# Optimization experiments

Hardware: AMD Instinct MI355X
Metric: run time of the kernel (lower is better)

## Reference

```python
import jax, jax.numpy as jnp
import numpy as np

B, N, D = 4, 4096, 512
H = 8
HD = D // H  # 64


def setup_inputs() -> dict:
    key = jax.random.key(0)
    ks = jax.random.split(key, 9)
    s = 1.0 / np.sqrt(D)
    return {
        "x": jax.random.normal(ks[0], (B, N, D), dtype=jnp.float32),
        "Wq": jax.random.normal(ks[1], (D, D), dtype=jnp.float32) * s,
        "bq": jax.random.normal(ks[2], (D,), dtype=jnp.float32) * 0.01,
        "Wk": jax.random.normal(ks[3], (D, D), dtype=jnp.float32) * s,
        "bk": jax.random.normal(ks[4], (D,), dtype=jnp.float32) * 0.01,
        "Wv": jax.random.normal(ks[5], (D, D), dtype=jnp.float32) * s,
        "bv": jax.random.normal(ks[6], (D,), dtype=jnp.float32) * 0.01,
        "Wo": jax.random.normal(ks[7], (D, D), dtype=jnp.float32) * s,
        "bo": jax.random.normal(ks[8], (D,), dtype=jnp.float32) * 0.01,
    }


def reference(x, Wq, bq, Wk, bk, Wv, bv, Wo, bo):
    # projections -> [B, H, N, HD]
    def split_heads(t):
        return t.reshape(B, N, H, HD).transpose(0, 2, 1, 3)

    q = split_heads(x @ Wq.T + bq)
    k = split_heads(x @ Wk.T + bk)
    v = split_heads(x @ Wv.T + bv)

    scale = 1.0 / np.sqrt(HD).astype(np.float32)
    scores = jnp.einsum("bhqd,bhkd->bhqk", q, k) * scale  # [B,H,N,N]
    attn = jax.nn.softmax(scores, axis=-1)
    out = jnp.einsum("bhqk,bhkd->bhqd", attn, v)  # [B,H,N,HD]
    out = out.transpose(0, 2, 1, 3).reshape(B, N, D)
    return out @ Wo.T + bo
```

## Files before the change

### kernel.cpp

```cpp
#include <hip/hip_runtime.h>
#include <hip/hip_bf16.h>

#define BB 4
#define NN 4096
#define DD 512
#define HH 8
#define HD 64

typedef __attribute__((ext_vector_type(4))) float f32x4;
typedef __attribute__((ext_vector_type(16))) float f32x16;
typedef __attribute__((ext_vector_type(8))) short short8;
typedef __attribute__((ext_vector_type(4))) unsigned int uint4v;

static __device__ __forceinline__ unsigned short f2bf(float f) {
    unsigned int u = __float_as_uint(f);
    u += 0x7fff + ((u >> 16) & 1);
    return (unsigned short)(u >> 16);
}

__global__ void convert_bf16(const float* __restrict__ in,
                             unsigned short* __restrict__ out, int n) {
    int i = (blockIdx.x * blockDim.x + threadIdx.x) * 8;
    int stride = gridDim.x * blockDim.x * 8;
    for (; i + 7 < n; i += stride) {
        f32x4 a = *reinterpret_cast<const f32x4*>(in + i);
        f32x4 b = *reinterpret_cast<const f32x4*>(in + i + 4);
        short8 o;
        o[0] = (short)f2bf(a[0]); o[1] = (short)f2bf(a[1]);
        o[2] = (short)f2bf(a[2]); o[3] = (short)f2bf(a[3]);
        o[4] = (short)f2bf(b[0]); o[5] = (short)f2bf(b[1]);
        o[6] = (short)f2bf(b[2]); o[7] = (short)f2bf(b[3]);
        *reinterpret_cast<short8*>(out + i) = o;
    }
}

__global__ void convert_weights(const float* __restrict__ W0, const float* __restrict__ W1,
                                const float* __restrict__ W2, const float* __restrict__ W3,
                                unsigned short* __restrict__ out) {
    int which = blockIdx.x >> 7;
    const float* src = which == 0 ? W0 : which == 1 ? W1 : which == 2 ? W2 : W3;
    unsigned short* dst = out + (size_t)which * DD * DD;
    int i = ((blockIdx.x & 127) * blockDim.x + threadIdx.x) * 8;
    f32x4 a = *reinterpret_cast<const f32x4*>(src + i);
    f32x4 b = *reinterpret_cast<const f32x4*>(src + i + 4);
    short8 o;
    o[0] = (short)f2bf(a[0]); o[1] = (short)f2bf(a[1]);
    o[2] = (short)f2bf(a[2]); o[3] = (short)f2bf(a[3]);
    o[4] = (short)f2bf(b[0]); o[5] = (short)f2bf(b[1]);
    o[6] = (short)f2bf(b[2]); o[7] = (short)f2bf(b[3]);
    *reinterpret_cast<short8*>(dst + i) = o;
}

template <int OUT_BF16>
__global__ __launch_bounds__(256)
void gemm_bias(const unsigned short* __restrict__ A,
               const unsigned short* __restrict__ W,
               const float* __restrict__ bias,
               void* __restrict__ Cout, float scale) {
    __shared__ uint4 ldsA[128 * 4];
    __shared__ uint4 ldsB[128 * 4];
    const int t = threadIdx.x;
    const int lane = t & 63;
    const int w = t >> 6;
    const int wr = w >> 1, wc = w & 1;
    const int brow = (int)blockIdx.y * 128;
    const int bcol = (int)blockIdx.x * 128;
    const int l16 = lane & 15;
    const int lq = lane >> 4;

    f32x4 acc[4][4] = {};

    const int sr = t >> 1;
    const int c16 = (t & 1) * 2;

    for (int k0 = 0; k0 < 512; k0 += 32) {
        const uint4* gA = reinterpret_cast<const uint4*>(A + (size_t)(brow + sr) * 512 + k0 + c16 * 8);
        const uint4* gB = reinterpret_cast<const uint4*>(W + (size_t)(bcol + sr) * 512 + k0 + c16 * 8);
        uint4 a0 = gA[0], a1 = gA[1];
        uint4 b0 = gB[0], b1 = gB[1];
        __syncthreads();
        ldsA[(sr * 4 + c16) ^ (sr & 7)]     = a0;
        ldsA[(sr * 4 + c16 + 1) ^ (sr & 7)] = a1;
        ldsB[(sr * 4 + c16) ^ (sr & 7)]     = b0;
        ldsB[(sr * 4 + c16 + 1) ^ (sr & 7)] = b1;
        __syncthreads();
        short8 af[4], bfr[4];
#pragma unroll
        for (int m = 0; m < 4; ++m) {
            int ra = wr * 64 + m * 16 + l16;
            af[m] = *reinterpret_cast<short8*>(&ldsA[(ra * 4 + lq) ^ (ra & 7)]);
            int rb = wc * 64 + m * 16 + l16;
            bfr[m] = *reinterpret_cast<short8*>(&ldsB[(rb * 4 + lq) ^ (rb & 7)]);
        }
#pragma unroll
        for (int m = 0; m < 4; ++m)
#pragma unroll
            for (int n = 0; n < 4; ++n)
                acc[m][n] = __builtin_amdgcn_mfma_f32_16x16x32_bf16(af[m], bfr[n], acc[m][n], 0, 0, 0);
    }

#pragma unroll
    for (int m = 0; m < 4; ++m) {
        int row = brow + wr * 64 + m * 16 + lq * 4;
#pragma unroll
        for (int n = 0; n < 4; ++n) {
            int col = bcol + wc * 64 + n * 16 + l16;
            float bv = bias[col];
#pragma unroll
            for (int r = 0; r < 4; ++r) {
                float v = (acc[m][n][r] + bv) * scale;
                if (OUT_BF16) {
                    ((unsigned short*)Cout)[(size_t)(row + r) * 512 + col] = f2bf(v);
                } else {
                    ((float*)Cout)[(size_t)(row + r) * 512 + col] = v;
                }
            }
        }
    }
}

__global__ __launch_bounds__(256)
void transpose_v(const unsigned short* __restrict__ Vb, unsigned short* __restrict__ Vt) {
    __shared__ unsigned short tile[64][72];
    const int bh = blockIdx.y;
    const int b = bh >> 3, h = bh & 7;
    const int n0 = blockIdx.x * 64;
    const int t = threadIdx.x;
    {
        int r = t >> 2;
        int cs = (t & 3) * 16;
        const short8* src = reinterpret_cast<const short8*>(
            Vb + (size_t)(b * NN + n0 + r) * DD + h * HD + cs);
        short8 v0 = src[0], v1 = src[1];
#pragma unroll
        for (int j = 0; j < 8; ++j) {
            tile[r][cs + j]     = (unsigned short)v0[j];
            tile[r][cs + 8 + j] = (unsigned short)v1[j];
        }
    }
    __syncthreads();
    {
        int d = t >> 2;
        int ns = (t & 3) * 16;
        short8 o0, o1;
#pragma unroll
        for (int j = 0; j < 8; ++j) {
            o0[j] = (short)tile[ns + j][d];
            o1[j] = (short)tile[ns + 8 + j][d];
        }
        unsigned short* dst = Vt + ((size_t)bh * HD + d) * NN + n0 + ns;
        *reinterpret_cast<short8*>(dst)     = o0;
        *reinterpret_cast<short8*>(dst + 8) = o1;
    }
}

__global__ __launch_bounds__(256)
void flash_attn(const unsigned short* __restrict__ Qb,
                const unsigned short* __restrict__ Kb,
                const unsigned short* __restrict__ Vt,
                unsigned short* __restrict__ Ob) {
    __shared__ __align__(16) char lds[32768];
    const int t = threadIdx.x;
    const int lane = t & 63;
    const int w = t >> 6;
    const int nid = (blockIdx.x & 7) * 128 + (blockIdx.x >> 3);
    const int bh = nid >> 5;
    const int qb = nid & 31;
    const int b = bh >> 3, h = bh & 7;
    const int q0 = qb * 128 + w * 32;
    const int l32 = lane & 31;
    const int hi = lane >> 5;

    const int i8 = lane >> 3, g8 = lane & 7;

    const unsigned short* qptr = Qb + (size_t)(b * NN + q0 + l32) * DD + h * HD + hi * 8;
    short8 qf[4];
#pragma unroll
    for (int c = 0; c < 4; ++c)
        qf[c] = *reinterpret_cast<const short8*>(qptr + c * 16);

    short8 ones;
#pragma unroll
    for (int j = 0; j < 8; ++j) ones[j] = (short)0x3F80;

    const f32x16 Z = {};
    f32x16 OT0 = {}, OT1 = {}, OTS = {};

    int koff[8], voff[8];
#pragma unroll
    for (int sub = 0; sub < 2; ++sub) {
#pragma unroll
        for (int c = 0; c < 4; ++c) {
            int row = sub * 32 + l32;
            int g = (hi + 2 * c) ^ (row & 7) ^ ((row >> 3) & 7);
            koff[sub * 4 + c] = row * 128 + g * 16;
        }
#pragma unroll
        for (int dblk = 0; dblk < 2; ++dblk)
#pragma unroll
            for (int c2 = 0; c2 < 2; ++c2) {
                int row = dblk * 32 + l32;
                int g = ((sub << 2) + (c2 << 1) + hi) ^ (row & 7) ^ ((row >> 3) & 7);
                voff[sub * 4 + dblk * 2 + c2] = 8192 + row * 128 + g * 16;
            }
    }

    const int rowl0 = w * 16 + i8;
    const int rowl1 = w * 16 + 8 + i8;
    const int gs0 = (g8 ^ i8 ^ ((2 * w) & 7)) * 8;
    const int gs1 = (g8 ^ i8 ^ ((2 * w + 1) & 7)) * 8;
    const unsigned short* kp0 = Kb + (size_t)(b * NN + rowl0) * DD + h * HD + gs0;
    const unsigned short* kp1 = Kb + (size_t)(b * NN + rowl1) * DD + h * HD + gs1;
    const unsigned short* vp0 = Vt + ((size_t)bh * HD + rowl0) * NN + gs0;
    const unsigned short* vp1 = Vt + ((size_t)bh * HD + rowl1) * NN + gs1;

    auto STAGE = [&](int bb) {
        __builtin_amdgcn_global_load_lds(
            (const __attribute__((address_space(1))) void*)kp0,
            (__attribute__((address_space(3))) void*)(lds + bb + (w * 16) * 128), 16, 0, 0);
        __builtin_amdgcn_global_load_lds(
            (const __attribute__((address_space(1))) void*)kp1,
            (__attribute__((address_space(3))) void*)(lds + bb + (w * 16 + 8) * 128), 16, 0, 0);
        __builtin_amdgcn_global_load_lds(
            (const __attribute__((address_space(1))) void*)vp0,
            (__attribute__((address_space(3))) void*)(lds + bb + 8192 + (w * 16) * 128), 16, 0, 0);
        __builtin_amdgcn_global_load_lds(
            (const __attribute__((address_space(1))) void*)vp1,
            (__attribute__((address_space(3))) void*)(lds + bb + 8192 + (w * 16 + 8) * 128), 16, 0, 0);
        kp0 += 64 * DD; kp1 += 64 * DD; vp0 += 64; vp1 += 64;
    };

    auto softpack = [&](const f32x16& S, short8& pa, short8& pb) {
        unsigned int wq[8];
#pragma unroll
        for (int j = 0; j < 8; ++j) {
            float p0 = __builtin_exp2f(S[2 * j]);
            float p1 = __builtin_exp2f(S[2 * j + 1]);
            asm("v_cvt_pk_bf16_f32 %0, %1, %2" : "=v"(wq[j]) : "v"(p0), "v"(p1));
        }
        asm("v_permlane32_swap_b32 %0, %1" : "+v"(wq[0]), "+v"(wq[2]));
        asm("v_permlane32_swap_b32 %0, %1" : "+v"(wq[1]), "+v"(wq[3]));
        asm("v_permlane32_swap_b32 %0, %1" : "+v"(wq[4]), "+v"(wq[6]));
        asm("v_permlane32_swap_b32 %0, %1" : "+v"(wq[5]), "+v"(wq[7]));
        uint4v pu0 = {wq[0], wq[1], wq[2], wq[3]};
        uint4v pu1 = {wq[4], wq[5], wq[6], wq[7]};
        pa = __builtin_bit_cast(short8, pu0);
        pb = __builtin_bit_cast(short8, pu1);
    };

    STAGE(0);
    __syncthreads();

    for (int it = 0; it < 32; ++it) {
#pragma unroll
        for (int half = 0; half < 2; ++half) {
            const int BO = half ? 16384 : 0;
            if (half == 0 || it != 31) STAGE(half ? 0 : 16384);

            short8 kf[8];
#pragma unroll
            for (int i = 0; i < 8; ++i)
                kf[i] = *reinterpret_cast<const short8*>(lds + BO + koff[i]);

            f32x16 S0, S1;
            S0 = __builtin_amdgcn_mfma_f32_32x32x16_bf16(kf[0], qf[0], Z, 0, 0, 0);
            S1 = __builtin_amdgcn_mfma_f32_32x32x16_bf16(kf[4], qf[0], Z, 0, 0, 0);
            S0 = __builtin_amdgcn_mfma_f32_32x32x16_bf16(kf[1], qf[1], S0, 0, 0, 0);
            S1 = __builtin_amdgcn_mfma_f32_32x32x16_bf16(kf[5], qf[1], S1, 0, 0, 0);
            S0 = __builtin_amdgcn_mfma_f32_32x32x16_bf16(kf[2], qf[2], S0, 0, 0, 0);
            S1 = __builtin_amdgcn_mfma_f32_32x32x16_bf16(kf[6], qf[2], S1, 0, 0, 0);
            S0 = __builtin_amdgcn_mfma_f32_32x32x16_bf16(kf[3], qf[3], S0, 0, 0, 0);
            S1 = __builtin_amdgcn_mfma_f32_32x32x16_bf16(kf[7], qf[3], S1, 0, 0, 0);

            short8 vf[8];
#pragma unroll
            for (int i = 0; i < 8; ++i)
                vf[i] = *reinterpret_cast<const short8*>(lds + BO + voff[i]);

            short8 p0a, p0b, p1a, p1b;
            softpack(S0, p0a, p0b);
            OT0 = __builtin_amdgcn_mfma_f32_32x32x16_bf16(vf[0], p0a, OT0, 0, 0, 0);
            OT0 = __builtin_amdgcn_mfma_f32_32x32x16_bf16(vf[1], p0b, OT0, 0, 0, 0);
            OT1 = __builtin_amdgcn_mfma_f32_32x32x16_bf16(vf[2], p0a, OT1, 0, 0, 0);
            OT1 = __builtin_amdgcn_mfma_f32_32x32x16_bf16(vf[3], p0b, OT1, 0, 0, 0);
            OTS = __builtin_amdgcn_mfma_f32_32x32x16_bf16(ones, p0a, OTS, 0, 0, 0);
            OTS = __builtin_amdgcn_mfma_f32_32x32x16_bf16(ones, p0b, OTS, 0, 0, 0);
            softpack(S1, p1a, p1b);
            OT0 = __builtin_amdgcn_mfma_f32_32x32x16_bf16(vf[4], p1a, OT0, 0, 0, 0);
            OT0 = __builtin_amdgcn_mfma_f32_32x32x16_bf16(vf[5], p1b, OT0, 0, 0, 0);
            OT1 = __builtin_amdgcn_mfma_f32_32x32x16_bf16(vf[6], p1a, OT1, 0, 0, 0);
            OT1 = __builtin_amdgcn_mfma_f32_32x32x16_bf16(vf[7], p1b, OT1, 0, 0, 0);
            OTS = __builtin_amdgcn_mfma_f32_32x32x16_bf16(ones, p1a, OTS, 0, 0, 0);
            OTS = __builtin_amdgcn_mfma_f32_32x32x16_bf16(ones, p1b, OTS, 0, 0, 0);

            __syncthreads();
        }
    }

    float inv = 1.0f / OTS[0];
    char* lw = lds + w * 4096;
#pragma unroll
    for (int dblk = 0; dblk < 2; ++dblk) {
#pragma unroll
        for (int g = 0; g < 4; ++g) {
#pragma unroll
            for (int j = 0; j < 2; ++j) {
                int r = 4 * g + 2 * j;
                int d = dblk * 32 + 8 * g + 2 * j + 4 * hi;
                float a = (dblk ? OT1[r] : OT0[r]) * inv;
                float bqv = (dblk ? OT1[r + 1] : OT0[r + 1]) * inv;
                unsigned int wv;
                asm("v_cvt_pk_bf16_f32 %0, %1, %2" : "=v"(wv) : "v"(a), "v"(bqv));
                int addr = (l32 * 128 + d * 2) ^ ((l32 & 7) << 4);
                *reinterpret_cast<unsigned int*>(lw + addr) = wv;
            }
        }
    }
#pragma unroll
    for (int it = 0; it < 4; ++it) {
        int q = lane >> 1;
        int seg = (lane & 1) + it * 2;
        uint4 val = *reinterpret_cast<uint4*>(lw + ((q * 128 + seg * 16) ^ ((q & 7) << 4)));
        *reinterpret_cast<uint4*>(Ob + (size_t)(b * NN + q0 + q) * DD + h * HD + seg * 8) = val;
    }
}

extern "C" void kernel_launch(void* const* d_in, const int* in_sizes, int n_in,
                              void* d_out, int out_size, void* d_ws, size_t ws_size,
                              hipStream_t stream) {
    (void)in_sizes; (void)n_in; (void)out_size; (void)ws_size;
    const float* x  = (const float*)d_in[0];
    const float* Wq = (const float*)d_in[1];
    const float* bq = (const float*)d_in[2];
    const float* Wk = (const float*)d_in[3];
    const float* bk = (const float*)d_in[4];
    const float* Wv = (const float*)d_in[5];
    const float* bv = (const float*)d_in[6];
    const float* Wo = (const float*)d_in[7];
    const float* bo = (const float*)d_in[8];
    float* out = (float*)d_out;

    char* ws = (char*)d_ws;
    const size_t BUF = 16777216;
    unsigned short* xb  = (unsigned short*)(ws);
    unsigned short* Qb  = (unsigned short*)(ws + BUF);
    unsigned short* Kb  = (unsigned short*)(ws + 2 * BUF);
    unsigned short* Vb  = (unsigned short*)(ws + 3 * BUF);
    unsigned short* Wqb = (unsigned short*)(ws + 4 * BUF);
    unsigned short* Wkb = Wqb + 262144;
    unsigned short* Wvb = Wkb + 262144;
    unsigned short* Wob = Wvb + 262144;
    unsigned short* Vt  = xb;
    unsigned short* Ob  = Vb;

    const int NTOK = BB * NN;
    const float cl = 0.125f * 1.4426950408889634f;

    convert_bf16<<<2048, 256, 0, stream>>>(x, xb, NTOK * DD);
    convert_weights<<<512, 256, 0, stream>>>(Wq, Wk, Wv, Wo, Wqb);

    dim3 ggrid(4, NTOK / 128);
    gemm_bias<1><<<ggrid, 256, 0, stream>>>(xb, Wqb, bq, Qb, cl);
    gemm_bias<1><<<ggrid, 256, 0, stream>>>(xb, Wkb, bk, Kb, 1.0f);
    gemm_bias<1><<<ggrid, 256, 0, stream>>>(xb, Wvb, bv, Vb, 1.0f);

    transpose_v<<<dim3(NN / 64, BB * HH), 256, 0, stream>>>(Vb, Vt);

    flash_attn<<<1024, 256, 0, stream>>>(Qb, Kb, Vt, Ob);

    gemm_bias<0><<<ggrid, 256, 0, stream>>>(Ob, Wob, bo, out, 1.0f);
}
```

Baseline: 304.8 us.

## Replace ones-MFMA row sum with scalar sums and use vmcnt-based double-buffer sync

```diff
diff --git a/kernel.cpp b/kernel.cpp
--- a/kernel.cpp
+++ b/kernel.cpp
@@ -179,12 +179,9 @@
     for (int c = 0; c < 4; ++c)
         qf[c] = *reinterpret_cast<const short8*>(qptr + c * 16);
 
-    short8 ones;
-#pragma unroll
-    for (int j = 0; j < 8; ++j) ones[j] = (short)0x3F80;
-
     const f32x16 Z = {};
-    f32x16 OT0 = {}, OT1 = {}, OTS = {};
+    f32x16 OT0 = {}, OT1 = {};
+    float lsum = 0.f;
 
     int koff[8], voff[8];
 #pragma unroll
@@ -236,6 +233,7 @@
         for (int j = 0; j < 8; ++j) {
             float p0 = __builtin_exp2f(S[2 * j]);
             float p1 = __builtin_exp2f(S[2 * j + 1]);
+            lsum += p0 + p1;
             asm("v_cvt_pk_bf16_f32 %0, %1, %2" : "=v"(wq[j]) : "v"(p0), "v"(p1));
         }
         asm("v_permlane32_swap_b32 %0, %1" : "+v"(wq[0]), "+v"(wq[2]));
@@ -248,56 +246,72 @@
         pb = __builtin_bit_cast(short8, pu1);
     };
 
+    auto COMPUTE = [&](int BO) {
+        short8 kf[8];
+#pragma unroll
+        for (int i = 0; i < 8; ++i)
+            kf[i] = *reinterpret_cast<const short8*>(lds + BO + koff[i]);
+
+        f32x16 S0, S1;
+        S0 = __builtin_amdgcn_mfma_f32_32x32x16_bf16(kf[0], qf[0], Z, 0, 0, 0);
+        S1 = __builtin_amdgcn_mfma_f32_32x32x16_bf16(kf[4], qf[0], Z, 0, 0, 0);
+        S0 = __builtin_amdgcn_mfma_f32_32x32x16_bf16(kf[1], qf[1], S0, 0, 0, 0);
+        S1 = __builtin_amdgcn_mfma_f32_32x32x16_bf16(kf[5], qf[1], S1, 0, 0, 0);
+        S0 = __builtin_amdgcn_mfma_f32_32x32x16_bf16(kf[2], qf[2], S0, 0, 0, 0);
+        S1 = __builtin_amdgcn_mfma_f32_32x32x16_bf16(kf[6], qf[2], S1, 0, 0, 0);
+        S0 = __builtin_amdgcn_mfma_f32_32x32x16_bf16(kf[3], qf[3], S0, 0, 0, 0);
+        S1 = __builtin_amdgcn_mfma_f32_32x32x16_bf16(kf[7], qf[3], S1, 0, 0, 0);
+
+        short8 vf[8];
+#pragma unroll
+        for (int i = 0; i < 8; ++i)
+            vf[i] = *reinterpret_cast<const short8*>(lds + BO + voff[i]);
+
+        short8 p0a, p0b, p1a, p1b;
+        softpack(S0, p0a, p0b);
+        OT0 = __builtin_amdgcn_mfma_f32_32x32x16_bf16(vf[0], p0a, OT0, 0, 0, 0);
+        OT0 = __builtin_amdgcn_mfma_f32_32x32x16_bf16(vf[1], p0b, OT0, 0, 0, 0);
+        OT1 = __builtin_amdgcn_mfma_f32_32x32x16_bf16(vf[2], p0a, OT1, 0, 0, 0);
+        OT1 = __builtin_amdgcn_mfma_f32_32x32x16_bf16(vf[3], p0b, OT1, 0, 0, 0);
+        softpack(S1, p1a, p1b);
+        OT0 = __builtin_amdgcn_mfma_f32_32x32x16_bf16(vf[4], p1a, OT0, 0, 0, 0);
+        OT0 = __builtin_amdgcn_mfma_f32_32x32x16_bf16(vf[5], p1b, OT0, 0, 0, 0);
+        OT1 = __builtin_amdgcn_mfma_f32_32x32x16_bf16(vf[6], p1a, OT1, 0, 0, 0);
+        OT1 = __builtin_amdgcn_mfma_f32_32x32x16_bf16(vf[7], p1b, OT1, 0, 0, 0);
+    };
+
     STAGE(0);
-    __syncthreads();
+    asm volatile("s_waitcnt vmcnt(0)" ::: "memory");
+    __builtin_amdgcn_s_barrier();
+    asm volatile("" ::: "memory");
 
     for (int it = 0; it < 32; ++it) {
-#pragma unroll
-        for (int half = 0; half < 2; ++half) {
-            const int BO = half ? 16384 : 0;
-            if (half == 0 || it != 31) STAGE(half ? 0 : 16384);
-
-            short8 kf[8];
-#pragma unroll
-            for (int i = 0; i < 8; ++i)
-                kf[i] = *reinterpret_cast<const short8*>(lds + BO + koff[i]);
-
-            f32x16 S0, S1;
-            S0 = __builtin_amdgcn_mfma_f32_32x32x16_bf16(kf[0], qf[0], Z, 0, 0, 0);
-            S1 = __builtin_amdgcn_mfma_f32_32x32x16_bf16(kf[4], qf[0], Z, 0, 0, 0);
-            S0 = __builtin_amdgcn_mfma_f32_32x32x16_bf16(kf[1], qf[1], S0, 0, 0, 0);
-            S1 = __builtin_amdgcn_mfma_f32_32x32x16_bf16(kf[5], qf[1], S1, 0, 0, 0);
-            S0 = __builtin_amdgcn_mfma_f32_32x32x16_bf16(kf[2], qf[2], S0, 0, 0, 0);
-            S1 = __builtin_amdgcn_mfma_f32_32x32x16_bf16(kf[6], qf[2], S1, 0, 0, 0);
-            S0 = __builtin_amdgcn_mfma_f32_32x32x16_bf16(kf[3], qf[3], S0, 0, 0, 0);
-            S1 = __builtin_amdgcn_mfma_f32_32x32x16_bf16(kf[7], qf[3], S1, 0, 0, 0);
-
-            short8 vf[8];
-#pragma unroll
-            for (int i = 0; i < 8; ++i)
-                vf[i] = *reinterpret_cast<const short8*>(lds + BO + voff[i]);
-
-            short8 p0a, p0b, p1a, p1b;
-            softpack(S0, p0a, p0b);
-            OT0 = __builtin_amdgcn_mfma_f32_32x32x16_bf16(vf[0], p0a, OT0, 0, 0, 0);
-            OT0 = __builtin_amdgcn_mfma_f32_32x32x16_bf16(vf[1], p0b, OT0, 0, 0, 0);
-            OT1 = __builtin_amdgcn_mfma_f32_32x32x16_bf16(vf[2], p0a, OT1, 0, 0, 0);
-            OT1 = __builtin_amdgcn_mfma_f32_32x32x16_bf16(vf[3], p0b, OT1, 0, 0, 0);
-            OTS = __builtin_amdgcn_mfma_f32_32x32x16_bf16(ones, p0a, OTS, 0, 0, 0);
-            OTS = __builtin_amdgcn_mfma_f32_32x32x16_bf16(ones, p0b, OTS, 0, 0, 0);
-            softpack(S1, p1a, p1b);
-            OT0 = __builtin_amdgcn_mfma_f32_32x32x16_bf16(vf[4], p1a, OT0, 0, 0, 0);
-            OT0 = __builtin_amdgcn_mfma_f32_32x32x16_bf16(vf[5], p1b, OT0, 0, 0, 0);
-            OT1 = __builtin_amdgcn_mfma_f32_32x32x16_bf16(vf[6], p1a, OT1, 0, 0, 0);
-            OT1 = __builtin_amdgcn_mfma_f32_32x32x16_bf16(vf[7], p1b, OT1, 0, 0, 0);
-            OTS = __builtin_amdgcn_mfma_f32_32x32x16_bf16(ones, p1a, OTS, 0, 0, 0);
-            OTS = __builtin_amdgcn_mfma_f32_32x32x16_bf16(ones, p1b, OTS, 0, 0, 0);
-
-            __syncthreads();
-        }
-    }
-
-    float inv = 1.0f / OTS[0];
+        STAGE(16384);
+        asm volatile("s_waitcnt vmcnt(4)" ::: "memory");
+        __builtin_amdgcn_s_barrier();
+        asm volatile("" ::: "memory");
+        COMPUTE(0);
+        asm volatile("" ::: "memory");
+        __builtin_amdgcn_s_barrier();
+        asm volatile("" ::: "memory");
+        if (it != 31) {
+            STAGE(0);
+            asm volatile("s_waitcnt vmcnt(4)" ::: "memory");
+        } else {
+            asm volatile("s_waitcnt vmcnt(0)" ::: "memory");
+        }
+        __builtin_amdgcn_s_barrier();
+        asm volatile("" ::: "memory");
+        COMPUTE(16384);
+        if (it != 31) {
+            asm volatile("" ::: "memory");
+            __builtin_amdgcn_s_barrier();
+            asm volatile("" ::: "memory");
+        }
+    }
+
+    lsum += __shfl_xor(lsum, 32);
+    float inv = 1.0f / lsum;
     char* lw = lds + w * 4096;
 #pragma unroll
     for (int dblk = 0; dblk < 2; ++dblk) {
```

Result: faster. 297.5 us (-2.4%).
